# Performance work log

Measured on AMD Instinct MI355X. Metric: run time of the kernel, lower is better.

## Reference

```python
import jax, jax.numpy as jnp
import numpy as np

B, N, C, H = 2, 2048, 768, 12
HD = C // H
SCALE = HD ** -0.5


def setup_inputs() -> dict:
    key = jax.random.key(0)
    k1, k2, k3, k4 = jax.random.split(key, 4)
    return {
        "x": jax.random.normal(k1, (B, N, C), dtype=jnp.float32),
        "qkv_w": jax.random.normal(k2, (3 * C, C), dtype=jnp.float32) * (C ** -0.5),
        "proj_w": jax.random.normal(k3, (C, C), dtype=jnp.float32) * (C ** -0.5),
        "proj_b": jax.random.normal(k4, (C,), dtype=jnp.float32) * 0.01,
    }


def reference(x, qkv_w, proj_w, proj_b):
    b, n, c = x.shape
    # qkv: Linear(dim, 3*dim, bias=False) -> (B,N,3,H,HD) -> per-tensor (B,H,N,HD)
    qkv = (x @ qkv_w.T).reshape(b, n, 3, H, HD)
    q, k, v = jnp.moveaxis(qkv, 2, 0)          # each (B,N,H,HD)
    q = q.transpose(0, 2, 1, 3)                # (B,H,N,HD)
    k = k.transpose(0, 2, 1, 3)
    v = v.transpose(0, 2, 1, 3)
    attn_logits = jnp.einsum("bhqd,bhkd->bhqk", q, k) * SCALE  # (B,H,N,N)
    attn = jax.nn.softmax(attn_logits, axis=-1)
    score = jnp.mean(attn, axis=1)             # (B,N,N) mean over heads
    # dropout p=0.0 -> identity
    out = jnp.einsum("bhqk,bhkd->bhqd", attn, v)  # (B,H,N,HD)
    out = out.transpose(0, 2, 1, 3).reshape(b, n, c)
    out = out @ proj_w.T + proj_b
    return out, score
```

## Files before the change

### kernel.cpp

```cpp
#include <hip/hip_runtime.h>
#include <cstddef>

typedef __attribute__((ext_vector_type(8))) short bf16x8;
typedef __attribute__((ext_vector_type(4))) float f32x4;

constexpr int Bb = 2, Nn = 2048, Cc = 768, Hh = 12, HDd = 64;
constexpr float QSCALE = 0.125f * 1.44269504088896340736f;

__device__ inline short f2bf(float f) {
  unsigned u = __builtin_bit_cast(unsigned, f);
  u += 0x7fff + ((u >> 16) & 1);
  return (short)(u >> 16);
}
__device__ inline unsigned cvtpk(float a, float b) {
  unsigned r;
  asm("v_cvt_pk_bf16_f32 %0, %1, %2" : "=v"(r) : "v"(a), "v"(b));
  return r;
}
__device__ inline void gl_lds16(const void* g, void* l) {
  __builtin_amdgcn_global_load_lds(
      (const __attribute__((address_space(1))) unsigned*)g,
      (__attribute__((address_space(3))) unsigned*)l, 16, 0, 0);
}
__device__ inline bf16x8 lds8(const short* p) { return *(const bf16x8*)p; }
__device__ inline bf16x8 ld_frag(const short* base, int row, int ch) {
  return *(const bf16x8*)&base[row * 64 + (((ch ^ (row & 7)) << 3))];
}

__global__ __launch_bounds__(256) void cvt_kernel(const float* __restrict__ s,
                                                  short* __restrict__ d) {
  const int i = (blockIdx.x * 256 + threadIdx.x) * 4;
  const float4 v = *(const float4*)&s[i];
  short4 o;
  o.x = f2bf(v.x); o.y = f2bf(v.y); o.z = f2bf(v.z); o.w = f2bf(v.w);
  *(short4*)&d[i] = o;
}

__global__ __launch_bounds__(256) void qkv_mfma(
    const short* __restrict__ A, const short* __restrict__ W,
    short* __restrict__ Qg, short* __restrict__ Kg, short* __restrict__ Vtg) {
  __shared__ short As[128 * 64];
  __shared__ short Bs[128 * 64];
  const int t = threadIdx.x, l = t & 63, w = t >> 6;
  const int lr = l & 15, lh = l >> 4;
  const int m0 = blockIdx.x * 128, r0 = blockIdx.y * 128;
  const int wr = w >> 1, wc = w & 1;
  f32x4 acc[4][4];
#pragma unroll
  for (int i = 0; i < 4; ++i)
#pragma unroll
    for (int j = 0; j < 4; ++j) acc[i][j] = (f32x4){0.f, 0.f, 0.f, 0.f};

  for (int k0 = 0; k0 < Cc; k0 += 64) {
    __syncthreads();
#pragma unroll
    for (int u = 0; u < 4; ++u) {
      const int du = (w * 4 + u) * 64 + l;
      const int row = du >> 3, ch = du & 7, sch = ch ^ (row & 7);
      gl_lds16(A + (size_t)(m0 + row) * Cc + k0 + sch * 8,
               &As[(w * 4 + u) * 512]);
      gl_lds16(W + (size_t)(r0 + row) * Cc + k0 + sch * 8,
               &Bs[(w * 4 + u) * 512]);
    }
    __syncthreads();
#pragma unroll
    for (int kp = 0; kp < 2; ++kp) {
      bf16x8 af[4], bfv[4];
#pragma unroll
      for (int i = 0; i < 4; ++i)
        af[i] = ld_frag(As, wr * 64 + i * 16 + lr, kp * 4 + lh);
#pragma unroll
      for (int j = 0; j < 4; ++j)
        bfv[j] = ld_frag(Bs, wc * 64 + j * 16 + lr, kp * 4 + lh);
#pragma unroll
      for (int i = 0; i < 4; ++i)
#pragma unroll
        for (int j = 0; j < 4; ++j)
          acc[i][j] = __builtin_amdgcn_mfma_f32_16x16x32_bf16(
              af[i], bfv[j], acc[i][j], 0, 0, 0);
    }
  }
  const int which = r0 / Cc;
  const int rbase = r0 % Cc;
  const int bq = m0 >> 11;
  const int nb = (m0 & 2047) + wr * 64;
  if (which == 2) {
#pragma unroll
    for (int j = 0; j < 4; ++j) {
      const int rr = rbase + wc * 64 + j * 16 + lr;
      const int head = rr >> 6, dd = rr & 63;
      short* vp = &Vtg[(((size_t)bq * Hh + head) * HDd + dd) * Nn];
#pragma unroll
      for (int i = 0; i < 4; ++i) {
        short4 o;
        o.x = f2bf(acc[i][j][0]); o.y = f2bf(acc[i][j][1]);
        o.z = f2bf(acc[i][j][2]); o.w = f2bf(acc[i][j][3]);
        *(short4*)&vp[nb + i * 16 + lh * 4] = o;
      }
    }
  } else {
    const float scl = (which == 0) ? QSCALE : 1.0f;
    short* __restrict__ dst = (which == 0) ? Qg : Kg;
#pragma unroll
    for (int j = 0; j < 4; ++j) {
      const int rr = rbase + wc * 64 + j * 16 + lr;
      const int head = rr >> 6, dd = rr & 63;
      short* dp = &dst[((size_t)bq * Hh + head) * Nn * HDd + dd];
#pragma unroll
      for (int i = 0; i < 4; ++i)
#pragma unroll
        for (int r = 0; r < 4; ++r)
          dp[(size_t)(nb + i * 16 + lh * 4 + r) * HDd] =
              f2bf(acc[i][j][r] * scl);
    }
  }
}

__global__ __launch_bounds__(256, 3) void attn_pass1(
    const short* __restrict__ Qg, const short* __restrict__ Kg,
    const short* __restrict__ Vtg, float* __restrict__ Linv,
    short* __restrict__ OHb) {
  __shared__ short SM[4 * 4096 + 4 * 1024];
  const int t = threadIdx.x, l = t & 63, w = t >> 6;
  const int lr = l & 15, lh = l >> 4;
  const int raw = blockIdx.x;
  const int bid = (raw & 7) * 96 + (raw >> 3);
  const int q0 = (bid & 31) * 64;
  const int head = (bid >> 5) % Hh;
  const int b = bid / (32 * Hh);
  const size_t base = (size_t)b * Hh + head;
  const short* Qh = Qg + base * Nn * HDd;
  const short* Kh = Kg + base * Nn * HDd;
  const short* Vh = Vtg + base * HDd * Nn;
  const int qw = q0 + w * 16;
  const int PB = 16384 + w * 1024;

  const bf16x8 onesf = {0x3F80, 0x3F80, 0x3F80, 0x3F80,
                        0x3F80, 0x3F80, 0x3F80, 0x3F80};

  int fof[2][4], wofi[4], pof[2];
#pragma unroll
  for (int kp = 0; kp < 2; ++kp) {
#pragma unroll
    for (int i = 0; i < 4; ++i)
      fof[kp][i] = (i * 16 + lr) * 64 + (((kp * 4 + lh) ^ (lr & 7)) << 3);
    pof[kp] = lr * 64 + (((kp * 4 + lh) ^ (lr & 7)) << 3);
  }
#pragma unroll
  for (int i = 0; i < 4; ++i) {
    const int ch = 2 * i + (lh >> 1);
    wofi[i] = lr * 64 + ((ch ^ (lr & 7)) << 3) + (lh & 1) * 4;
  }

  bf16x8 qf[2];
#pragma unroll
  for (int kp = 0; kp < 2; ++kp)
    qf[kp] = *(const bf16x8*)&Qh[(size_t)(qw + lr) * HDd + kp * 32 + lh * 8];

  f32x4 accO[4], accL;
  accL = (f32x4){0.f, 0.f, 0.f, 0.f};
#pragma unroll
  for (int j = 0; j < 4; ++j) accO[j] = (f32x4){0.f, 0.f, 0.f, 0.f};

  auto stageK = [&](const int kb, const int tile) {
    const short* Kt = Kh + (size_t)tile * (64 * HDd);
#pragma unroll
    for (int u = 0; u < 2; ++u) {
      const int cu = u * 4 + w;
      const int du = cu * 64 + l;
      const int row = du >> 3, ch = du & 7, sch = ch ^ (row & 7);
      gl_lds16(Kt + row * 64 + sch * 8, &SM[kb + cu * 512]);
    }
  };
  auto stageV = [&](const int vb, const int tile) {
    const short* Vt = Vh + tile * 64;
#pragma unroll
    for (int u = 0; u < 2; ++u) {
      const int cu = u * 4 + w;
      const int du = cu * 64 + l;
      const int row = du >> 3, ch = du & 7, sch = ch ^ (row & 7);
      gl_lds16(Vt + (size_t)row * Nn + sch * 8, &SM[vb + cu * 512]);
    }
  };

  auto qk = [&](const int kb, f32x4 (&sacc)[4]) {
#pragma unroll
    for (int i = 0; i < 4; ++i) sacc[i] = (f32x4){0.f, 0.f, 0.f, 0.f};
#pragma unroll
    for (int kp = 0; kp < 2; ++kp)
#pragma unroll
      for (int i = 0; i < 4; ++i)
        sacc[i] = __builtin_amdgcn_mfma_f32_16x16x32_bf16(
            lds8(&SM[kb + fof[kp][i]]), qf[kp], sacc[i], 0, 0, 0);
  };
  auto expw = [&](const f32x4 (&sacc)[4]) {
#pragma unroll
    for (int i = 0; i < 4; ++i) {
      const float p0 = exp2f(sacc[i][0]), p1 = exp2f(sacc[i][1]);
      const float p2 = exp2f(sacc[i][2]), p3 = exp2f(sacc[i][3]);
      uint2 pk;
      pk.x = cvtpk(p0, p1);
      pk.y = cvtpk(p2, p3);
      *(uint2*)&SM[PB + wofi[i]] = pk;
    }
  };
  auto pv = [&](const int vb) {
#pragma unroll
    for (int kp = 0; kp < 2; ++kp) {
      const bf16x8 pa = lds8(&SM[PB + pof[kp]]);
      accL = __builtin_amdgcn_mfma_f32_16x16x32_bf16(pa, onesf, accL, 0, 0, 0);
#pragma unroll
      for (int j = 0; j < 4; ++j)
        accO[j] = __builtin_amdgcn_mfma_f32_16x16x32_bf16(
            pa, lds8(&SM[vb + fof[kp][j]]), accO[j], 0, 0, 0);
    }
  };

  f32x4 sA[4], sB[4];
  stageK(0, 0);
  __syncthreads();
  stageK(4096, 1);
  stageV(8192, 0);
  qk(0, sA);
  __syncthreads();
#pragma unroll 1
  for (int it = 1; it < 31; it += 2) {
    stageK(0, it + 1);
    stageV(12288, it);
    qk(4096, sB);
    expw(sA);
    pv(8192);
    __syncthreads();
    stageK(4096, it + 2);
    stageV(8192, it + 1);
    qk(0, sA);
    expw(sB);
    pv(12288);
    __syncthreads();
  }
  stageV(12288, 31);
  qk(4096, sB);
  expw(sA);
  pv(8192);
  __syncthreads();
  expw(sB);
  pv(12288);

  f32x4 linvq;
#pragma unroll
  for (int r = 0; r < 4; ++r) linvq[r] = 1.0f / accL[r];
  if (lr == 0) *(f32x4*)&Linv[base * Nn + qw + 4 * lh] = linvq;
#pragma unroll
  for (int j = 0; j < 4; ++j)
#pragma unroll
    for (int r = 0; r < 4; ++r)
      OHb[((size_t)b * Nn + qw + 4 * lh + r) * Cc + head * HDd + j * 16 + lr] =
          f2bf(accO[j][r] * linvq[r]);
}

__global__ __launch_bounds__(256, 4) void score_mfma(
    const short* __restrict__ Qg, const short* __restrict__ Kg,
    const float* __restrict__ Linv, float* __restrict__ score) {
  __shared__ __align__(16) char SMraw[64 * 68 * 4];
  short* SK = (short*)SMraw;
  float* SMf = (float*)SMraw;
  const int t = threadIdx.x, l = t & 63, w = t >> 6;
  const int lr = l & 15, lh = l >> 4;
  const int raw = blockIdx.x;
  const int xcd = raw & 7, idx = raw >> 3;
  const int b = xcd >> 2;
  const int q0 = ((xcd & 3) * 8 + (idx >> 5)) * 64;
  const int kv0 = (idx & 31) * 64;
  const int qw = q0 + w * 16;

  int fof[2][4];
#pragma unroll
  for (int kp = 0; kp < 2; ++kp)
#pragma unroll
    for (int i = 0; i < 4; ++i)
      fof[kp][i] = (i * 16 + lr) * 64 + (((kp * 4 + lh) ^ (lr & 7)) << 3);

  f32x4 sc[4];
#pragma unroll
  for (int i = 0; i < 4; ++i) sc[i] = (f32x4){0.f, 0.f, 0.f, 0.f};

  auto stage = [&](const int kb, const int h) {
    const short* Kt = Kg + (((size_t)b * Hh + h) * Nn + kv0) * HDd;
#pragma unroll
    for (int u = 0; u < 2; ++u) {
      const int cu = u * 4 + w;
      const int du = cu * 64 + l;
      const int row = du >> 3, ch = du & 7, sch = ch ^ (row & 7);
      gl_lds16(Kt + row * 64 + sch * 8, &SK[kb + cu * 512]);
    }
  };
  auto ldqQ = [&](const int h, bf16x8& a0, bf16x8& a1) {
    const size_t hb = (size_t)b * Hh + h;
    a0 = *(const bf16x8*)&Qg[(hb * Nn + qw + lr) * HDd + lh * 8];
    a1 = *(const bf16x8*)&Qg[(hb * Nn + qw + lr) * HDd + 32 + lh * 8];
  };
  auto qk = [&](const int kb, const bf16x8 a0, const bf16x8 a1,
                f32x4 (&sacc)[4]) {
#pragma unroll
    for (int i = 0; i < 4; ++i) sacc[i] = (f32x4){0.f, 0.f, 0.f, 0.f};
#pragma unroll
    for (int i = 0; i < 4; ++i)
      sacc[i] = __builtin_amdgcn_mfma_f32_16x16x32_bf16(
          lds8(&SK[kb + fof[0][i]]), a0, sacc[i], 0, 0, 0);
#pragma unroll
    for (int i = 0; i < 4; ++i)
      sacc[i] = __builtin_amdgcn_mfma_f32_16x16x32_bf16(
          lds8(&SK[kb + fof[1][i]]), a1, sacc[i], 0, 0, 0);
  };
  auto expacc = [&](const f32x4 (&sacc)[4], const float lv) {
#pragma unroll
    for (int i = 0; i < 4; ++i)
#pragma unroll
      for (int r = 0; r < 4; ++r) sc[i][r] += exp2f(sacc[i][r]) * lv;
  };

  bf16x8 qA0, qA1, qB0, qB1;
  float lvA, lvB;
  f32x4 sA[4], sB[4];
  stage(0, 0);
  ldqQ(0, qA0, qA1);
  __syncthreads();
  stage(4096, 1);
  ldqQ(1, qB0, qB1);
  lvA = Linv[((size_t)b * Hh + 0) * Nn + qw + lr];
  qk(0, qA0, qA1, sA);
  __syncthreads();
#pragma unroll 1
  for (int h = 1; h < 11; h += 2) {
    stage(0, h + 1);
    ldqQ(h + 1, qA0, qA1);
    lvB = Linv[((size_t)b * Hh + h) * Nn + qw + lr];
    qk(4096, qB0, qB1, sB);
    expacc(sA, lvA);
    __syncthreads();
    stage(4096, h + 2);
    ldqQ(h + 2, qB0, qB1);
    lvA = Linv[((size_t)b * Hh + h + 1) * Nn + qw + lr];
    qk(0, qA0, qA1, sA);
    expacc(sB, lvB);
    __syncthreads();
  }
  lvB = Linv[((size_t)b * Hh + 11) * Nn + qw + lr];
  qk(4096, qB0, qB1, sB);
  expacc(sA, lvA);
  expacc(sB, lvB);
  __syncthreads();

  constexpr float invH = 1.0f / 12.0f;
#pragma unroll
  for (int i = 0; i < 4; ++i) {
    f32x4 o;
#pragma unroll
    for (int r = 0; r < 4; ++r) o[r] = sc[i][r] * invH;
    *(f32x4*)&SMf[(w * 16 + lr) * 68 + i * 16 + 4 * lh] = o;
  }
  __syncthreads();
#pragma unroll
  for (int s = 0; s < 4; ++s) {
    const int lin = t + s * 256;
    const int row = lin >> 4, ch = lin & 15;
    const f32x4 v = *(const f32x4*)&SMf[row * 68 + ch * 4];
    *(f32x4*)&score[((size_t)b * Nn + q0 + row) * Nn + kv0 + ch * 4] = v;
  }
}

__global__ __launch_bounds__(256) void proj_mfma(
    const short* __restrict__ A, const short* __restrict__ W,
    const float* __restrict__ bias, float* __restrict__ out) {
  __shared__ short As[128 * 64];
  __shared__ short Bs[128 * 64];
  const int t = threadIdx.x, l = t & 63, w = t >> 6;
  const int lr = l & 15, lh = l >> 4;
  const int m0 = blockIdx.x * 128, c0 = blockIdx.y * 128;
  const int wr = w >> 1, wc = w & 1;
  f32x4 acc[4][4];
#pragma unroll
  for (int i = 0; i < 4; ++i)
#pragma unroll
    for (int j = 0; j < 4; ++j) acc[i][j] = (f32x4){0.f, 0.f, 0.f, 0.f};

  for (int k0 = 0; k0 < Cc; k0 += 64) {
    __syncthreads();
#pragma unroll
    for (int u = 0; u < 4; ++u) {
      const int du = (w * 4 + u) * 64 + l;
      const int row = du >> 3, ch = du & 7, sch = ch ^ (row & 7);
      gl_lds16(A + (size_t)(m0 + row) * Cc + k0 + sch * 8,
               &As[(w * 4 + u) * 512]);
      gl_lds16(W + (size_t)(c0 + row) * Cc + k0 + sch * 8,
               &Bs[(w * 4 + u) * 512]);
    }
    __syncthreads();
#pragma unroll
    for (int kp = 0; kp < 2; ++kp) {
      bf16x8 af[4], bfv[4];
#pragma unroll
      for (int i = 0; i < 4; ++i)
        af[i] = ld_frag(As, wr * 64 + i * 16 + lr, kp * 4 + lh);
#pragma unroll
      for (int j = 0; j < 4; ++j)
        bfv[j] = ld_frag(Bs, wc * 64 + j * 16 + lr, kp * 4 + lh);
#pragma unroll
      for (int i = 0; i < 4; ++i)
#pragma unroll
        for (int j = 0; j < 4; ++j)
          acc[i][j] = __builtin_amdgcn_mfma_f32_16x16x32_bf16(
              af[i], bfv[j], acc[i][j], 0, 0, 0);
    }
  }
#pragma unroll
  for (int j = 0; j < 4; ++j) {
    const int c = c0 + wc * 64 + j * 16 + lr;
    const float bi = bias[c];
#pragma unroll
    for (int i = 0; i < 4; ++i)
#pragma unroll
      for (int r = 0; r < 4; ++r) {
        const int m = m0 + wr * 64 + i * 16 + lh * 4 + r;
        out[(size_t)m * Cc + c] = acc[i][j][r] + bi;
      }
  }
}

extern "C" void kernel_launch(void* const* d_in, const int* in_sizes, int n_in,
                              void* d_out, int out_size, void* d_ws,
                              size_t ws_size, hipStream_t stream) {
  const float* x = (const float*)d_in[0];
  const float* qkv_w = (const float*)d_in[1];
  const float* proj_w = (const float*)d_in[2];
  const float* proj_b = (const float*)d_in[3];

  float* out = (float*)d_out;
  float* score = out + (size_t)Bb * Nn * Cc;

  const size_t nx = (size_t)Bb * Nn * Cc;
  const size_t nwq = (size_t)3 * Cc * Cc;
  const size_t npw = (size_t)Cc * Cc;
  short* xb = (short*)d_ws;
  short* wqb = xb + nx;
  short* pwb = wqb + nwq;
  short* Qb = pwb + npw;
  short* Kb = Qb + nx;
  short* Vtb = Kb + nx;
  short* OHb = Vtb + nx;
  float* Linv = (float*)(OHb + nx);

  cvt_kernel<<<dim3((int)(nx / 1024)), 256, 0, stream>>>(x, xb);
  cvt_kernel<<<dim3((int)(nwq / 1024)), 256, 0, stream>>>(qkv_w, wqb);
  cvt_kernel<<<dim3((int)(npw / 1024)), 256, 0, stream>>>(proj_w, pwb);
  qkv_mfma<<<dim3(32, 18), 256, 0, stream>>>(xb, wqb, Qb, Kb, Vtb);
  attn_pass1<<<dim3(768), 256, 0, stream>>>(Qb, Kb, Vtb, Linv, OHb);
  score_mfma<<<dim3(2048), 256, 0, stream>>>(Qb, Kb, Linv, score);
  proj_mfma<<<dim3(32, 6), 256, 0, stream>>>(OHb, pwb, proj_b, out);
}
```

Measured before the change: 143.9 us.

## Double-buffer QKV GEMM and restructure attention pipeline with vmcnt waits

The QKV GEMM now double-buffers its LDS tiles, prefetching the next K-slice while computing the current one. The attention kernel's staggered K/V staging is replaced by a simpler two-buffer scheme. Both use explicit s_waitcnt vmcnt with raw barriers instead of __syncthreads, and s_setprio raises wave priority around MFMA blocks. This is meant to hide global-load latency, at the cost of doubling GEMM LDS use, which may lower occupancy. The attention restructure also drops the previous QK/PV software skew between tiles, so less work may overlap.

```diff
diff --git a/kernel.cpp b/kernel.cpp
--- a/kernel.cpp
+++ b/kernel.cpp
@@ -6,6 +6,9 @@
 
 constexpr int Bb = 2, Nn = 2048, Cc = 768, Hh = 12, HDd = 64;
 constexpr float QSCALE = 0.125f * 1.44269504088896340736f;
+
+#define VMCNT(n) asm volatile("s_waitcnt vmcnt(" #n ")" ::: "memory")
+#define SBAR() __builtin_amdgcn_s_barrier()
 
 __device__ inline short f2bf(float f) {
   unsigned u = __builtin_bit_cast(unsigned, f);
@@ -39,8 +42,8 @@
 __global__ __launch_bounds__(256) void qkv_mfma(
     const short* __restrict__ A, const short* __restrict__ W,
     short* __restrict__ Qg, short* __restrict__ Kg, short* __restrict__ Vtg) {
-  __shared__ short As[128 * 64];
-  __shared__ short Bs[128 * 64];
+  __shared__ short As[2 * 8192];
+  __shared__ short Bs[2 * 8192];
   const int t = threadIdx.x, l = t & 63, w = t >> 6;
   const int lr = l & 15, lh = l >> 4;
   const int m0 = blockIdx.x * 128, r0 = blockIdx.y * 128;
@@ -51,35 +54,59 @@
 #pragma unroll
     for (int j = 0; j < 4; ++j) acc[i][j] = (f32x4){0.f, 0.f, 0.f, 0.f};
 
-  for (int k0 = 0; k0 < Cc; k0 += 64) {
-    __syncthreads();
+  auto stage = [&](const int buf, const int kt) {
 #pragma unroll
     for (int u = 0; u < 4; ++u) {
       const int du = (w * 4 + u) * 64 + l;
       const int row = du >> 3, ch = du & 7, sch = ch ^ (row & 7);
-      gl_lds16(A + (size_t)(m0 + row) * Cc + k0 + sch * 8,
-               &As[(w * 4 + u) * 512]);
-      gl_lds16(W + (size_t)(r0 + row) * Cc + k0 + sch * 8,
-               &Bs[(w * 4 + u) * 512]);
-    }
-    __syncthreads();
+      gl_lds16(A + (size_t)(m0 + row) * Cc + kt * 64 + sch * 8,
+               &As[buf * 8192 + (w * 4 + u) * 512]);
+      gl_lds16(W + (size_t)(r0 + row) * Cc + kt * 64 + sch * 8,
+               &Bs[buf * 8192 + (w * 4 + u) * 512]);
+    }
+  };
+  auto compute = [&](const int buf) {
+    const short* Ab = As + buf * 8192;
+    const short* Bbp = Bs + buf * 8192;
 #pragma unroll
     for (int kp = 0; kp < 2; ++kp) {
       bf16x8 af[4], bfv[4];
 #pragma unroll
       for (int i = 0; i < 4; ++i)
-        af[i] = ld_frag(As, wr * 64 + i * 16 + lr, kp * 4 + lh);
+        af[i] = ld_frag(Ab, wr * 64 + i * 16 + lr, kp * 4 + lh);
 #pragma unroll
       for (int j = 0; j < 4; ++j)
-        bfv[j] = ld_frag(Bs, wc * 64 + j * 16 + lr, kp * 4 + lh);
+        bfv[j] = ld_frag(Bbp, wc * 64 + j * 16 + lr, kp * 4 + lh);
+      __builtin_amdgcn_s_setprio(1);
 #pragma unroll
       for (int i = 0; i < 4; ++i)
 #pragma unroll
         for (int j = 0; j < 4; ++j)
           acc[i][j] = __builtin_amdgcn_mfma_f32_16x16x32_bf16(
               af[i], bfv[j], acc[i][j], 0, 0, 0);
-    }
-  }
+      __builtin_amdgcn_s_setprio(0);
+    }
+  };
+
+  stage(0, 0);
+#pragma unroll 1
+  for (int kk = 0; kk < 10; kk += 2) {
+    stage(1, kk + 1);
+    VMCNT(8); SBAR();
+    compute(0);
+    SBAR();
+    stage(0, kk + 2);
+    VMCNT(8); SBAR();
+    compute(1);
+    SBAR();
+  }
+  stage(1, 11);
+  VMCNT(8); SBAR();
+  compute(0);
+  SBAR();
+  VMCNT(0); SBAR();
+  compute(1);
+
   const int which = r0 / Cc;
   const int rbase = r0 % Cc;
   const int bq = m0 >> 11;
@@ -162,38 +189,33 @@
 #pragma unroll
   for (int j = 0; j < 4; ++j) accO[j] = (f32x4){0.f, 0.f, 0.f, 0.f};
 
-  auto stageK = [&](const int kb, const int tile) {
+  auto stage = [&](const int buf, const int tile) {
     const short* Kt = Kh + (size_t)tile * (64 * HDd);
+    const short* Vt = Vh + tile * 64;
 #pragma unroll
     for (int u = 0; u < 2; ++u) {
       const int cu = u * 4 + w;
       const int du = cu * 64 + l;
       const int row = du >> 3, ch = du & 7, sch = ch ^ (row & 7);
-      gl_lds16(Kt + row * 64 + sch * 8, &SM[kb + cu * 512]);
-    }
-  };
-  auto stageV = [&](const int vb, const int tile) {
-    const short* Vt = Vh + tile * 64;
-#pragma unroll
-    for (int u = 0; u < 2; ++u) {
-      const int cu = u * 4 + w;
-      const int du = cu * 64 + l;
-      const int row = du >> 3, ch = du & 7, sch = ch ^ (row & 7);
-      gl_lds16(Vt + (size_t)row * Nn + sch * 8, &SM[vb + cu * 512]);
-    }
-  };
-
-  auto qk = [&](const int kb, f32x4 (&sacc)[4]) {
+      gl_lds16(Kt + row * 64 + sch * 8, &SM[buf * 4096 + cu * 512]);
+      gl_lds16(Vt + (size_t)row * Nn + sch * 8,
+               &SM[8192 + buf * 4096 + cu * 512]);
+    }
+  };
+
+  auto compute = [&](const int kb) {
+    const int vb = 8192 + kb;
+    f32x4 sacc[4];
 #pragma unroll
     for (int i = 0; i < 4; ++i) sacc[i] = (f32x4){0.f, 0.f, 0.f, 0.f};
+    __builtin_amdgcn_s_setprio(1);
 #pragma unroll
     for (int kp = 0; kp < 2; ++kp)
 #pragma unroll
       for (int i = 0; i < 4; ++i)
         sacc[i] = __builtin_amdgcn_mfma_f32_16x16x32_bf16(
             lds8(&SM[kb + fof[kp][i]]), qf[kp], sacc[i], 0, 0, 0);
-  };
-  auto expw = [&](const f32x4 (&sacc)[4]) {
+    __builtin_amdgcn_s_setprio(0);
 #pragma unroll
     for (int i = 0; i < 4; ++i) {
       const float p0 = exp2f(sacc[i][0]), p1 = exp2f(sacc[i][1]);
@@ -203,8 +225,7 @@
       pk.y = cvtpk(p2, p3);
       *(uint2*)&SM[PB + wofi[i]] = pk;
     }
-  };
-  auto pv = [&](const int vb) {
+    __builtin_amdgcn_s_setprio(1);
 #pragma unroll
     for (int kp = 0; kp < 2; ++kp) {
       const bf16x8 pa = lds8(&SM[PB + pof[kp]]);
@@ -214,37 +235,27 @@
         accO[j] = __builtin_amdgcn_mfma_f32_16x16x32_bf16(
             pa, lds8(&SM[vb + fof[kp][j]]), accO[j], 0, 0, 0);
     }
-  };
-
-  f32x4 sA[4], sB[4];
-  stageK(0, 0);
-  __syncthreads();
-  stageK(4096, 1);
-  stageV(8192, 0);
-  qk(0, sA);
-  __syncthreads();
+    __builtin_amdgcn_s_setprio(0);
+  };
+
+  stage(0, 0);
 #pragma unroll 1
-  for (int it = 1; it < 31; it += 2) {
-    stageK(0, it + 1);
-    stageV(12288, it);
-    qk(4096, sB);
-    expw(sA);
-    pv(8192);
-    __syncthreads();
-    stageK(4096, it + 2);
-    stageV(8192, it + 1);
-    qk(0, sA);
-    expw(sB);
-    pv(12288);
-    __syncthreads();
-  }
-  stageV(12288, 31);
-  qk(4096, sB);
-  expw(sA);
-  pv(8192);
-  __syncthreads();
-  expw(sB);
-  pv(12288);
+  for (int it = 0; it < 30; it += 2) {
+    stage(1, it + 1);
+    VMCNT(4); SBAR();
+    compute(0);
+    SBAR();
+    stage(0, it + 2);
+    VMCNT(4); SBAR();
+    compute(4096);
+    SBAR();
+  }
+  stage(1, 31);
+  VMCNT(4); SBAR();
+  compute(0);
+  SBAR();
+  VMCNT(0); SBAR();
+  compute(4096);
 
   f32x4 linvq;
 #pragma unroll
```

Result: no change. 141.2 us (-1.9%).
